# Optimization experiments

Measured on AMD Instinct MI355X. Metric: run time of the kernel, lower is better.

The kernel has to match this reference:

```python
import jax, jax.numpy as jnp
import numpy as np

EMBED_PHI = 1024
EMBED_F = 1024
HIDDEN_F = 1024
N_HEADS = 16
B, S = 2, 2048


def setup_inputs() -> dict:
    key = jax.random.key(0)
    ks = jax.random.split(key, 9)
    sphi = 1.0 / np.sqrt(EMBED_PHI)
    sf = 1.0 / np.sqrt(EMBED_F)
    sh = 1.0 / np.sqrt(HIDDEN_F)
    return {
        "q": jax.random.normal(ks[0], (B, S, EMBED_PHI), jnp.float32),
        "k": jax.random.normal(ks[1], (B, S, EMBED_PHI), jnp.float32),
        "v": jax.random.normal(ks[2], (B, S, EMBED_F), jnp.float32),
        "Wq": jax.random.normal(ks[3], (HIDDEN_F, EMBED_PHI), jnp.float32) * sphi,
        "Wk": jax.random.normal(ks[4], (HIDDEN_F, EMBED_PHI), jnp.float32) * sphi,
        "Wv": jax.random.normal(ks[5], (HIDDEN_F, EMBED_F), jnp.float32) * sf,
        "bv": jax.random.normal(ks[6], (HIDDEN_F,), jnp.float32) * sf,
        "Wo": jax.random.normal(ks[7], (EMBED_F, HIDDEN_F), jnp.float32) * sh,
        "bo": jax.random.normal(ks[8], (EMBED_F,), jnp.float32) * sh,
    }


def reference(q, k, v, Wq, Wk, Wv, bv, Wo, bo):
    Bq, Sq, _ = q.shape
    hd = HIDDEN_F // N_HEADS
    scale = 1.0 / np.sqrt(hd)
    # projections; torch Linear: y = x @ W.T + b
    qh = (q @ Wq.T).reshape(Bq, Sq, N_HEADS, hd).transpose(0, 2, 1, 3)  # [B,H,S,d]
    kh = (k @ Wk.T).reshape(Bq, Sq, N_HEADS, hd).transpose(0, 2, 1, 3)
    vh = (v @ Wv.T + bv).reshape(Bq, Sq, N_HEADS, hd).transpose(0, 2, 1, 3)
    scores = jnp.einsum("bhsd,bhtd->bhst", qh, kh) * scale  # [B,H,S,S]
    # mask: triu(diagonal=0) masked (attend strictly to past) except [0,0] unmasked
    mask = jnp.triu(jnp.ones((Sq, Sq), dtype=bool), k=0).at[0, 0].set(False)
    scores = jnp.where(mask, -jnp.inf, scores)
    probs = jax.nn.softmax(scores, axis=-1)  # dropout is identity at eval
    out = jnp.einsum("bhst,bhtd->bhsd", probs, vh)
    out = out.transpose(0, 2, 1, 3).reshape(Bq, Sq, HIDDEN_F)
    return out @ Wo.T + bo
```

## Files before the change

### kernel.cpp

```cpp
#include <hip/hip_runtime.h>
#include <hip/hip_bf16.h>

typedef __attribute__((ext_vector_type(8))) short short8;
typedef __attribute__((ext_vector_type(4))) float f32x4;
typedef __attribute__((ext_vector_type(4))) unsigned short us4;

#define NE  1024
#define SEQ 2048

__device__ __forceinline__ float bf2f(unsigned short u) {
    union { unsigned u; float f; } x; x.u = ((unsigned)u) << 16; return x.f;
}
__device__ __forceinline__ unsigned short f2bf(float f) {
    union { float f; unsigned u; } x; x.f = f;
    unsigned r = x.u + 0x7FFFu + ((x.u >> 16) & 1u);
    return (unsigned short)(r >> 16);
}
__device__ __forceinline__ unsigned short f2bf_fast(float f) {
    union { float f; unsigned u; } x; x.f = f;
    return (unsigned short)((x.u + 0x8000u) >> 16);
}

__global__ void detect_dtype(const unsigned short* __restrict__ s,
                             int* __restrict__ flag) {
    __shared__ int cnt;
    const int t = threadIdx.x;
    if (t == 0) cnt = 0;
    __syncthreads();
    unsigned short u = s[t];
    int e = (u >> 7) & 0xFF;
    int sane = (e == 0) || (e >= 100 && e <= 140);
    atomicAdd(&cnt, sane);
    __syncthreads();
    if (t == 0) flag[0] = (cnt >= 230) ? 1 : 0;
}

struct Ptrs7 { const void* s[7]; unsigned short* d[7]; };

__global__ void convert7(Ptrs7 p, const int* __restrict__ flag, int zoff) {
    const int z = blockIdx.z + zoff;
    const int n = (z < 3) ? (4 << 20) : (1 << 20);
    const bool in_f32 = (flag[0] == 0);
    unsigned short* d = p.d[z];
    const int stride = gridDim.x * blockDim.x;
    for (int i8 = blockIdx.x * blockDim.x + threadIdx.x; i8 * 8 < n; i8 += stride) {
        size_t off = (size_t)i8 * 8;
        if (in_f32) {
            const float* sp = (const float*)p.s[z] + off;
            float4 a = *(const float4*)sp, b2 = *(const float4*)(sp + 4);
            short8 sv;
            sv[0] = (short)f2bf(a.x);  sv[1] = (short)f2bf(a.y);
            sv[2] = (short)f2bf(a.z);  sv[3] = (short)f2bf(a.w);
            sv[4] = (short)f2bf(b2.x); sv[5] = (short)f2bf(b2.y);
            sv[6] = (short)f2bf(b2.z); sv[7] = (short)f2bf(b2.w);
            *(short8*)(d + off) = sv;
        } else {
            *(short8*)(d + off) = *(const short8*)((const unsigned short*)p.s[z] + off);
        }
    }
}

template<int AWS, int WWS, int OUTF, int VT>
__global__ __launch_bounds__(256, 3)
void gemm_bt(const void* A0, const void* A1, const void* A2,
             const void* W0, const void* W1, const void* W2,
             const void* b0, const void* b1, const void* b2,
             void* C0, void* C1, void* C2,
             const int* __restrict__ flag)
{
    __shared__ __align__(16) unsigned short As[128 * 32];
    __shared__ __align__(16) unsigned short Bs[128 * 32];
    const int z = blockIdx.z;
    const void* Ap = (z == 0) ? A0 : (z == 1) ? A1 : A2;
    const void* Wp = (z == 0) ? W0 : (z == 1) ? W1 : W2;
    const void* bp = (z == 0) ? b0 : (z == 1) ? b1 : b2;
    void*       Cp = (z == 0) ? C0 : (z == 1) ? C1 : C2;
    const bool in_f32 = (flag[0] == 0);
    const int t = threadIdx.x;
    const int w = t >> 6, l = t & 63, q = l >> 4, n = l & 15;
    const int m0 = blockIdx.y * 128, n0 = blockIdx.x * 128;
    const int wm = (w >> 1) * 64, wn = (w & 1) * 64;
    const int srow = t >> 2, sk = (t & 3) * 8;

    f32x4 acc[4][4] = {};

    for (int k0 = 0; k0 < NE; k0 += 32) {
        if (AWS || !in_f32) {
            #pragma unroll
            for (int hh = 0; hh < 2; hh++) {
                const unsigned short* ga = (const unsigned short*)Ap +
                    (size_t)(m0 + srow + hh * 64) * NE + k0 + sk;
                __builtin_amdgcn_global_load_lds(
                    (const __attribute__((address_space(1))) void*)ga,
                    (__attribute__((address_space(3))) void*)&As[hh * 2048 + w * 512],
                    16, 0, 0);
            }
        } else {
            #pragma unroll
            for (int hh = 0; hh < 2; hh++) {
                const float* a = (const float*)Ap +
                                 (size_t)(m0 + srow + hh * 64) * NE + k0 + sk;
                float4 x0 = *(const float4*)a, x1 = *(const float4*)(a + 4);
                short8 sv;
                sv[0] = (short)f2bf(x0.x); sv[1] = (short)f2bf(x0.y);
                sv[2] = (short)f2bf(x0.z); sv[3] = (short)f2bf(x0.w);
                sv[4] = (short)f2bf(x1.x); sv[5] = (short)f2bf(x1.y);
                sv[6] = (short)f2bf(x1.z); sv[7] = (short)f2bf(x1.w);
                *(short8*)(&As[hh * 2048 + t * 8]) = sv;
            }
        }
        if (WWS || !in_f32) {
            #pragma unroll
            for (int hh = 0; hh < 2; hh++) {
                const unsigned short* ga = (const unsigned short*)Wp +
                    (size_t)(n0 + srow + hh * 64) * NE + k0 + sk;
                __builtin_amdgcn_global_load_lds(
                    (const __attribute__((address_space(1))) void*)ga,
                    (__attribute__((address_space(3))) void*)&Bs[hh * 2048 + w * 512],
                    16, 0, 0);
            }
        } else {
            #pragma unroll
            for (int hh = 0; hh < 2; hh++) {
                const float* a = (const float*)Wp +
                                 (size_t)(n0 + srow + hh * 64) * NE + k0 + sk;
                float4 x0 = *(const float4*)a, x1 = *(const float4*)(a + 4);
                short8 sv;
                sv[0] = (short)f2bf(x0.x); sv[1] = (short)f2bf(x0.y);
                sv[2] = (short)f2bf(x0.z); sv[3] = (short)f2bf(x0.w);
                sv[4] = (short)f2bf(x1.x); sv[5] = (short)f2bf(x1.y);
                sv[6] = (short)f2bf(x1.z); sv[7] = (short)f2bf(x1.w);
                *(short8*)(&Bs[hh * 2048 + t * 8]) = sv;
            }
        }
        __syncthreads();

        short8 af[4], bfv[4];
        #pragma unroll
        for (int mt = 0; mt < 4; mt++)
            af[mt] = *(const short8*)(&As[(wm + mt * 16 + n) * 32 + q * 8]);
        #pragma unroll
        for (int nt = 0; nt < 4; nt++)
            bfv[nt] = *(const short8*)(&Bs[(wn + nt * 16 + n) * 32 + q * 8]);
        #pragma unroll
        for (int mt = 0; mt < 4; mt++)
            #pragma unroll
            for (int nt = 0; nt < 4; nt++)
                acc[mt][nt] = __builtin_amdgcn_mfma_f32_16x16x32_bf16(
                    af[mt], bfv[nt], acc[mt][nt], 0, 0, 0);
        __syncthreads();
    }

    #pragma unroll
    for (int mt = 0; mt < 4; mt++)
        #pragma unroll
        for (int nt = 0; nt < 4; nt++) {
            int row0 = m0 + wm + mt * 16 + q * 4;
            int col  = n0 + wn + nt * 16 + n;
            float bia = 0.f;
            if (bp)
                bia = in_f32 ? ((const float*)bp)[col]
                             : bf2f(((const unsigned short*)bp)[col]);
            if (VT && z == 2) {
                int bb = row0 >> 11, s0 = row0 & 2047;
                int hh2 = col >> 6, dd = col & 63;
                us4 pk4;
                #pragma unroll
                for (int r = 0; r < 4; r++)
                    pk4[r] = f2bf(acc[mt][nt][r] + bia);
                *(us4*)((unsigned short*)Cp +
                        ((size_t)((bb * 16 + hh2) * 64 + dd) << 11) + s0) = pk4;
            } else {
                #pragma unroll
                for (int r = 0; r < 4; r++) {
                    float v2 = acc[mt][nt][r] + bia;
                    size_t idx = (size_t)(row0 + r) * NE + col;
                    if (OUTF && in_f32) ((float*)Cp)[idx] = v2;
                    else                ((unsigned short*)Cp)[idx] = f2bf(v2);
                }
            }
        }
}

__global__ __launch_bounds__(256, 3)
void attn(const unsigned short* qh, const unsigned short* kh,
          const unsigned short* vt, unsigned short* ctx)
{
    __shared__ __align__(16) unsigned short Ks[128 * 72];
    __shared__ __align__(16) unsigned short Vt[64 * 136];
    __shared__ __align__(16) unsigned short Ps[4][16 * 72];
    const int t = threadIdx.x, w = t >> 6, l = t & 63;
    const int q = l >> 4, n = l & 15;
    const int qb = 31 - blockIdx.x;
    const int h = blockIdx.y, b = blockIdx.z;
    const size_t base = (size_t)b * SEQ * NE + h * 64;
    const size_t vbase = (size_t)((b * 16 + h) * 64) << 11;
    const int i0 = qb * 64 + w * 16;

    short8 qf[2];
    qf[0] = *(const short8*)(&qh[base + (size_t)(i0 + n) * NE + q * 8]);
    qf[1] = *(const short8*)(&qh[base + (size_t)(i0 + n) * NE + 32 + q * 8]);

    f32x4 o[4] = {};
    float ls[4] = {0.f, 0.f, 0.f, 0.f};

    const float K1 = 0.125f * 1.4426950408889634f;
    const float B2 = 24.0f * 1.4426950408889634f;

    const int jtmax = qb >> 1;
    short8 pk[4], pv[4];
    #pragma unroll
    for (int i = 0; i < 4; i++) {
        int c = t + i * 256;
        pk[i] = *(const short8*)(&kh[base + (size_t)(c >> 3) * NE + (c & 7) * 8]);
        pv[i] = *(const short8*)(&vt[vbase + ((size_t)(c >> 4) << 11) + (c & 15) * 8]);
    }

    unsigned short* PsW = &Ps[w][0];

    for (int jt = 0; jt <= jtmax; jt++) {
        #pragma unroll
        for (int i = 0; i < 4; i++) {
            int c = t + i * 256;
            *(short8*)(&Ks[(c >> 3) * 72 + (c & 7) * 8]) = pk[i];
            *(short8*)(&Vt[(c >> 4) * 136 + (c & 15) * 8]) = pv[i];
        }
        __syncthreads();

        if (jt < jtmax) {
            const int jn = (jt + 1) * 128;
            #pragma unroll
            for (int i = 0; i < 4; i++) {
                int c = t + i * 256;
                pk[i] = *(const short8*)(&kh[base + (size_t)(jn + (c >> 3)) * NE + (c & 7) * 8]);
                pv[i] = *(const short8*)(&vt[vbase + ((size_t)(c >> 4) << 11) + jn + (c & 15) * 8]);
            }
        }

        #pragma unroll
        for (int khalf = 0; khalf < 2; khalf++) {
            const int kstart = jt * 128 + khalf * 64;
            if (kstart > qb * 64) break;
            const bool diag = (kstart == qb * 64);
            const int kloc = khalf * 64;

            f32x4 sa[4] = {};
            #pragma unroll
            for (int ks = 0; ks < 2; ks++)
                #pragma unroll
                for (int nt = 0; nt < 4; nt++) {
                    short8 kf = *(const short8*)(&Ks[(kloc + nt * 16 + n) * 72 + ks * 32 + q * 8]);
                    sa[nt] = __builtin_amdgcn_mfma_f32_16x16x32_bf16(qf[ks], kf, sa[nt], 0, 0, 0);
                }

            #pragma unroll
            for (int nt = 0; nt < 4; nt++)
                #pragma unroll
                for (int r = 0; r < 4; r++) {
                    float e = fmaf(sa[nt][r], K1, -B2);
                    if (diag) {
                        int j = kstart + nt * 16 + n;
                        int i = i0 + q * 4 + r;
                        bool ok = (j < i) || (i == 0 && j == 0);
                        e = ok ? e : -256.0f;
                    }
                    float p = __builtin_amdgcn_exp2f(e);
                    ls[r] += p;
                    PsW[(q * 4 + r) * 72 + nt * 16 + n] = f2bf_fast(p);
                }
            asm volatile("s_waitcnt lgkmcnt(0)" ::: "memory");

            #pragma unroll
            for (int ks = 0; ks < 2; ks++) {
                short8 pf = *(const short8*)(&PsW[n * 72 + ks * 32 + q * 8]);
                #pragma unroll
                for (int dt = 0; dt < 4; dt++) {
                    short8 vf = *(const short8*)(&Vt[(dt * 16 + n) * 136 + kloc + ks * 32 + q * 8]);
                    o[dt] = __builtin_amdgcn_mfma_f32_16x16x32_bf16(pf, vf, o[dt], 0, 0, 0);
                }
            }
            asm volatile("" ::: "memory");
        }
        __syncthreads();
    }

    #pragma unroll
    for (int r = 0; r < 4; r++)
        #pragma unroll
        for (int xm = 1; xm <= 8; xm <<= 1)
            ls[r] += __shfl_xor(ls[r], xm, 64);

    #pragma unroll
    for (int r = 0; r < 4; r++) {
        float inv = 1.0f / ls[r];
        #pragma unroll
        for (int dt = 0; dt < 4; dt++)
            ctx[base + (size_t)(i0 + q * 4 + r) * NE + dt * 16 + n] =
                f2bf(o[dt][r] * inv);
    }
}

extern "C" void kernel_launch(void* const* d_in, const int* in_sizes, int n_in,
                              void* d_out, int out_size, void* d_ws, size_t ws_size,
                              hipStream_t stream) {
    const void* q  = d_in[0];
    const void* k  = d_in[1];
    const void* v  = d_in[2];
    const void* Wq = d_in[3];
    const void* Wk = d_in[4];
    const void* Wv = d_in[5];
    const void* bv = d_in[6];
    const void* Wo = d_in[7];
    const void* bo = d_in[8];

    const size_t MB = 1024 * 1024;
    const size_t M4 = 4 * MB;
    unsigned short* ws = (unsigned short*)d_ws;
    unsigned short* qh  = ws;
    unsigned short* kh  = ws + 1 * M4;
    unsigned short* vt  = ws + 2 * M4;
    unsigned short* ctx = qh;

    int tier = (ws_size >= 56 * MB + 64) ? 2 : (ws_size >= 32 * MB + 64) ? 1 : 0;

    unsigned short *qc, *kc, *vc, *Wqc, *Wkc, *Wvc, *Woc;
    int* flag;
    if (tier == 2) {
        qc = ws + 3 * M4; kc = ws + 4 * M4; vc = ws + 5 * M4;
        Wqc = ws + 6 * M4;           Wkc = Wqc + 1 * MB;
        Wvc = Wqc + 2 * MB;          Woc = Wqc + 3 * MB;
        flag = (int*)((char*)d_ws + 56 * MB);
    } else if (tier == 1) {
        qc = kc = vc = nullptr;
        Wqc = ws + 3 * M4;           Wkc = Wqc + 1 * MB;
        Wvc = Wqc + 2 * MB;          Woc = Wqc + 3 * MB;
        flag = (int*)((char*)d_ws + 32 * MB);
    } else {
        qc = kc = vc = nullptr; Wqc = Wkc = Wvc = Woc = nullptr;
        flag = (int*)((char*)d_ws + 24 * MB);
    }

    detect_dtype<<<1, 256, 0, stream>>>((const unsigned short*)q, flag);

    if (tier > 0) {
        Ptrs7 p;
        p.s[0] = q;  p.s[1] = k;  p.s[2] = v;
        p.s[3] = Wq; p.s[4] = Wk; p.s[5] = Wv; p.s[6] = Wo;
        p.d[0] = qc; p.d[1] = kc; p.d[2] = vc;
        p.d[3] = Wqc; p.d[4] = Wkc; p.d[5] = Wvc; p.d[6] = Woc;
        if (tier == 2)
            convert7<<<dim3(512, 1, 7), 256, 0, stream>>>(p, flag, 0);
        else
            convert7<<<dim3(512, 1, 4), 256, 0, stream>>>(p, flag, 3);
    }

    if (tier == 2)
        gemm_bt<1, 1, 0, 1><<<dim3(8, 32, 3), 256, 0, stream>>>(
            qc, kc, vc, Wqc, Wkc, Wvc, nullptr, nullptr, bv, qh, kh, vt, flag);
    else if (tier == 1)
        gemm_bt<0, 1, 0, 1><<<dim3(8, 32, 3), 256, 0, stream>>>(
            q, k, v, Wqc, Wkc, Wvc, nullptr, nullptr, bv, qh, kh, vt, flag);
    else
        gemm_bt<0, 0, 0, 1><<<dim3(8, 32, 3), 256, 0, stream>>>(
            q, k, v, Wq, Wk, Wv, nullptr, nullptr, bv, qh, kh, vt, flag);

    attn<<<dim3(32, 16, 2), 256, 0, stream>>>(qh, kh, vt, ctx);

    if (tier > 0)
        gemm_bt<1, 1, 1, 0><<<dim3(8, 32, 1), 256, 0, stream>>>(
            ctx, ctx, ctx, Woc, Woc, Woc, bo, bo, bo, d_out, d_out, d_out, flag);
    else
        gemm_bt<1, 0, 1, 0><<<dim3(8, 32, 1), 256, 0, stream>>>(
            ctx, ctx, ctx, Wo, Wo, Wo, bo, bo, bo, d_out, d_out, d_out, flag);
}
```

Baseline: 258.0 us.

## Pair complementary causal query blocks per workgroup sharing K/V tiles

The attention kernel now launches 512-thread workgroups that each handle two query blocks, qb and 31-qb. The two blocks share the same streamed K/V tiles, which balances causal work across workgroups and halves the number of workgroups. The K/V tile drops from 128 to 64 keys per iteration, so there are more iterations and more barriers, and the shorter block's half sits idle after it finishes its own tiles. Launch bounds change to 512 threads with an occupancy hint of 4.

```diff
diff --git a/kernel.cpp b/kernel.cpp
--- a/kernel.cpp
+++ b/kernel.cpp
@@ -182,20 +182,23 @@
         }
 }
 
-__global__ __launch_bounds__(256, 3)
+__global__ __launch_bounds__(512, 4)
 void attn(const unsigned short* qh, const unsigned short* kh,
           const unsigned short* vt, unsigned short* ctx)
 {
-    __shared__ __align__(16) unsigned short Ks[128 * 72];
-    __shared__ __align__(16) unsigned short Vt[64 * 136];
-    __shared__ __align__(16) unsigned short Ps[4][16 * 72];
+    __shared__ __align__(16) unsigned short Ks[64 * 72];
+    __shared__ __align__(16) unsigned short Vt[64 * 72];
+    __shared__ __align__(16) unsigned short Ps[8][16 * 72];
     const int t = threadIdx.x, w = t >> 6, l = t & 63;
     const int q = l >> 4, n = l & 15;
-    const int qb = 31 - blockIdx.x;
+    const int half = w >> 2, sub = w & 3;
+    const int pair = blockIdx.x;
+    const int qbB = pair, qbA = 31 - pair;
+    const int qb = half ? qbB : qbA;
     const int h = blockIdx.y, b = blockIdx.z;
     const size_t base = (size_t)b * SEQ * NE + h * 64;
     const size_t vbase = (size_t)((b * 16 + h) * 64) << 11;
-    const int i0 = qb * 64 + w * 16;
+    const int i0 = qb * 64 + sub * 16;
 
     short8 qf[2];
     qf[0] = *(const short8*)(&qh[base + (size_t)(i0 + n) * NE + q * 8]);
@@ -207,59 +210,44 @@
     const float K1 = 0.125f * 1.4426950408889634f;
     const float B2 = 24.0f * 1.4426950408889634f;
 
-    const int jtmax = qb >> 1;
-    short8 pk[4], pv[4];
-    #pragma unroll
-    for (int i = 0; i < 4; i++) {
-        int c = t + i * 256;
-        pk[i] = *(const short8*)(&kh[base + (size_t)(c >> 3) * NE + (c & 7) * 8]);
-        pv[i] = *(const short8*)(&vt[vbase + ((size_t)(c >> 4) << 11) + (c & 15) * 8]);
-    }
+    const int kr = t >> 3, kc = (t & 7) * 8;
+    const int vd = t >> 3, vj = (t & 7) * 8;
+
+    short8 pk, pv;
+    pk = *(const short8*)(&kh[base + (size_t)kr * NE + kc]);
+    pv = *(const short8*)(&vt[vbase + ((size_t)vd << 11) + vj]);
 
     unsigned short* PsW = &Ps[w][0];
 
-    for (int jt = 0; jt <= jtmax; jt++) {
-        #pragma unroll
-        for (int i = 0; i < 4; i++) {
-            int c = t + i * 256;
-            *(short8*)(&Ks[(c >> 3) * 72 + (c & 7) * 8]) = pk[i];
-            *(short8*)(&Vt[(c >> 4) * 136 + (c & 15) * 8]) = pv[i];
-        }
+    for (int jt = 0; jt <= qbA; jt++) {
+        *(short8*)(&Ks[kr * 72 + kc]) = pk;
+        *(short8*)(&Vt[vd * 72 + vj]) = pv;
         __syncthreads();
 
-        if (jt < jtmax) {
-            const int jn = (jt + 1) * 128;
-            #pragma unroll
-            for (int i = 0; i < 4; i++) {
-                int c = t + i * 256;
-                pk[i] = *(const short8*)(&kh[base + (size_t)(jn + (c >> 3)) * NE + (c & 7) * 8]);
-                pv[i] = *(const short8*)(&vt[vbase + ((size_t)(c >> 4) << 11) + jn + (c & 15) * 8]);
-            }
-        }
-
-        #pragma unroll
-        for (int khalf = 0; khalf < 2; khalf++) {
-            const int kstart = jt * 128 + khalf * 64;
-            if (kstart > qb * 64) break;
-            const bool diag = (kstart == qb * 64);
-            const int kloc = khalf * 64;
-
+        if (jt < qbA) {
+            const int jn = (jt + 1) * 64;
+            pk = *(const short8*)(&kh[base + (size_t)(jn + kr) * NE + kc]);
+            pv = *(const short8*)(&vt[vbase + ((size_t)vd << 11) + jn + vj]);
+        }
+
+        if (jt <= qb) {
             f32x4 sa[4] = {};
             #pragma unroll
             for (int ks = 0; ks < 2; ks++)
                 #pragma unroll
                 for (int nt = 0; nt < 4; nt++) {
-                    short8 kf = *(const short8*)(&Ks[(kloc + nt * 16 + n) * 72 + ks * 32 + q * 8]);
+                    short8 kf = *(const short8*)(&Ks[(nt * 16 + n) * 72 + ks * 32 + q * 8]);
                     sa[nt] = __builtin_amdgcn_mfma_f32_16x16x32_bf16(qf[ks], kf, sa[nt], 0, 0, 0);
                 }
 
+            const bool diag = (jt == qb);
             #pragma unroll
             for (int nt = 0; nt < 4; nt++)
                 #pragma unroll
                 for (int r = 0; r < 4; r++) {
                     float e = fmaf(sa[nt][r], K1, -B2);
                     if (diag) {
-                        int j = kstart + nt * 16 + n;
+                        int j = jt * 64 + nt * 16 + n;
                         int i = i0 + q * 4 + r;
                         bool ok = (j < i) || (i == 0 && j == 0);
                         e = ok ? e : -256.0f;
@@ -275,11 +263,10 @@
                 short8 pf = *(const short8*)(&PsW[n * 72 + ks * 32 + q * 8]);
                 #pragma unroll
                 for (int dt = 0; dt < 4; dt++) {
-                    short8 vf = *(const short8*)(&Vt[(dt * 16 + n) * 136 + kloc + ks * 32 + q * 8]);
+                    short8 vf = *(const short8*)(&Vt[(dt * 16 + n) * 72 + ks * 32 + q * 8]);
                     o[dt] = __builtin_amdgcn_mfma_f32_16x16x32_bf16(pf, vf, o[dt], 0, 0, 0);
                 }
             }
-            asm volatile("" ::: "memory");
         }
         __syncthreads();
     }
@@ -364,7 +351,7 @@
         gemm_bt<0, 0, 0, 1><<<dim3(8, 32, 3), 256, 0, stream>>>(
             q, k, v, Wq, Wk, Wv, nullptr, nullptr, bv, qh, kh, vt, flag);
 
-    attn<<<dim3(32, 16, 2), 256, 0, stream>>>(qh, kh, vt, ctx);
+    attn<<<dim3(16, 16, 2), 512, 0, stream>>>(qh, kh, vt, ctx);
 
     if (tier > 0)
         gemm_bt<1, 1, 1, 0><<<dim3(8, 32, 1), 256, 0, stream>>>(
```

Result: faster. 229.7 us (-11.0%).
